# Performance work log

Measured on AMD Instinct MI355X. Metric: run time of the kernel, lower is better.

The kernel has to match this reference:

```python
import jax, jax.numpy as jnp
import numpy as np

HEADS = 8

def setup_inputs() -> dict:
    key = jax.random.key(0)
    ks = jax.random.split(key, 5)
    B, C, H, W = 2, 256, 64, 64
    dim = C
    x = jax.random.normal(ks[0], (B, C, H, W), dtype=jnp.float32)
    # Linear weights stored as [in, out] so y = x @ W + b
    w_qkv = jax.random.normal(ks[1], (dim, 3 * dim), dtype=jnp.float32) * (dim ** -0.5)
    b_qkv = jax.random.normal(ks[2], (3 * dim,), dtype=jnp.float32) * 0.02
    w_out = jax.random.normal(ks[3], (dim, dim), dtype=jnp.float32) * (dim ** -0.5)
    b_out = jax.random.normal(ks[4], (dim,), dtype=jnp.float32) * 0.02
    return {"x": x, "w_qkv": w_qkv, "b_qkv": b_qkv, "w_out": w_out, "b_out": b_out}

def reference(x, w_qkv, b_qkv, w_out, b_out):
    B, C, H, W = x.shape
    h = HEADS
    d = C // h
    scale = d ** -0.5
    # [B, C, H, W] -> [B, N, C]
    tokens = x.reshape(B, C, H * W).transpose(0, 2, 1)
    qkv = tokens @ w_qkv + b_qkv  # [B, N, 3C]
    q, k, v = jnp.split(qkv, 3, axis=-1)
    def to_heads(t):
        Bn, N, _ = t.shape
        return t.reshape(Bn, N, h, d).transpose(0, 2, 1, 3)  # [B, h, N, d]
    q, k, v = map(to_heads, (q, k, v))
    dots = jnp.einsum('bhnd,bhmd->bhnm', q, k) * scale  # [B, h, N, N]
    attn = jax.nn.softmax(dots, axis=-1)
    out = jnp.einsum('bhnm,bhmd->bhnd', attn, v)  # [B, h, N, d]
    out = out.transpose(0, 2, 1, 3).reshape(B, H * W, C)  # [B, N, C]
    out = out @ w_out + b_out
    return out.transpose(0, 2, 1).reshape(B, C, H, W)
```

## Files before the change

kernel.cpp:

```cpp
#include <hip/hip_runtime.h>

typedef __attribute__((ext_vector_type(8))) short s16x8;
typedef __attribute__((ext_vector_type(4))) short s16x4;
typedef __attribute__((ext_vector_type(4))) float f32x4;
typedef __attribute__((ext_vector_type(2))) unsigned u32x2;

#define MFMA32(a, b, c) __builtin_amdgcn_mfma_f32_16x16x32_bf16((a), (b), (c), 0, 0, 0)

#if __has_builtin(__builtin_amdgcn_mfma_f32_16x16x16bf16_1k)
#define HAVE_MFMA16 1
#define MFMA16K(a, b, c) __builtin_amdgcn_mfma_f32_16x16x16bf16_1k((a), (b), (c), 0, 0, 0)
#elif __has_builtin(__builtin_amdgcn_mfma_f32_16x16x16_bf16)
#define HAVE_MFMA16 1
#define MFMA16K(a, b, c) __builtin_amdgcn_mfma_f32_16x16x16_bf16((a), (b), (c), 0, 0, 0)
#else
#define HAVE_MFMA16 0
#endif

#if __has_builtin(__builtin_amdgcn_exp2f)
#define EXP2F(x) __builtin_amdgcn_exp2f(x)
#else
#define EXP2F(x) __exp2f(x)
#endif

#define SL2E 0.25507313f

__device__ __forceinline__ unsigned pkrne(float a, float b) {
  unsigned ua = __builtin_bit_cast(unsigned, a);
  unsigned ub = __builtin_bit_cast(unsigned, b);
  ua += 0x7FFFu + ((ua >> 16) & 1u);
  ub += 0x7FFFu + ((ub >> 16) & 1u);
  return __builtin_amdgcn_perm(ub, ua, 0x07060302u);
}

__device__ __forceinline__ unsigned pktrunc(float a, float b) {
  return __builtin_amdgcn_perm(__builtin_bit_cast(unsigned, b),
                               __builtin_bit_cast(unsigned, a), 0x07060302u);
}

__device__ __forceinline__ unsigned short bfr(float f) {
  unsigned u = __builtin_bit_cast(unsigned, f);
  u += 0x7FFFu + ((u >> 16) & 1u);
  return (unsigned short)(u >> 16);
}

__global__ __launch_bounds__(256) void prep_kernel(
    const float* __restrict__ x, const float* __restrict__ wqkv,
    const float* __restrict__ wout, ushort* __restrict__ xbf,
    ushort* __restrict__ wT, ushort* __restrict__ woT) {
  const int t = threadIdx.x;
  const int sub = t & 15, grp = t >> 4;
  const int id = blockIdx.x;
  const float* src;
  ushort* dst;
  int src_ld, k0, n0;
  float sc = 1.f;
  if (id < 512) {
    int mt = id & 63, kt = (id >> 6) & 3, b = id >> 8;
    src = x + (size_t)b * 256 * 4096;
    src_ld = 4096;
    dst = xbf + (size_t)b * 4096 * 256;
    k0 = kt * 64;
    n0 = mt * 64;
  } else if (id < 560) {
    int r = id - 512, nt = r % 12, kt = r / 12;
    src = wqkv;
    src_ld = 768;
    dst = wT;
    k0 = kt * 64;
    n0 = nt * 64;
    if (n0 < 256) sc = SL2E;
  } else {
    int r = id - 560, nt = r & 3, kt = r >> 2;
    src = wout;
    src_ld = 256;
    dst = woT;
    k0 = kt * 64;
    n0 = nt * 64;
  }
  const int k = k0 + grp * 4;
  const int n = n0 + sub * 4;
  unsigned d0[4], d1[4];
#pragma unroll
  for (int i = 0; i < 4; ++i) {
    float4 v = *(const float4*)(src + (size_t)(k + i) * src_ld + n);
    d0[i] = pkrne(v.x * sc, v.y * sc);
    d1[i] = pkrne(v.z * sc, v.w * sc);
  }
  u32x2 r0 = {__builtin_amdgcn_perm(d0[1], d0[0], 0x05040100u),
              __builtin_amdgcn_perm(d0[3], d0[2], 0x05040100u)};
  u32x2 r1 = {__builtin_amdgcn_perm(d0[1], d0[0], 0x07060302u),
              __builtin_amdgcn_perm(d0[3], d0[2], 0x07060302u)};
  u32x2 r2 = {__builtin_amdgcn_perm(d1[1], d1[0], 0x05040100u),
              __builtin_amdgcn_perm(d1[3], d1[2], 0x05040100u)};
  u32x2 r3 = {__builtin_amdgcn_perm(d1[1], d1[0], 0x07060302u),
              __builtin_amdgcn_perm(d1[3], d1[2], 0x07060302u)};
  *(u32x2*)(dst + (size_t)(n + 0) * 256 + k) = r0;
  *(u32x2*)(dst + (size_t)(n + 1) * 256 + k) = r1;
  *(u32x2*)(dst + (size_t)(n + 2) * 256 + k) = r2;
  *(u32x2*)(dst + (size_t)(n + 3) * 256 + k) = r3;
}

__global__ __launch_bounds__(256) void qkv_kernel(
    const ushort* __restrict__ xbf, const ushort* __restrict__ wT,
    const float* __restrict__ bq, ushort* __restrict__ QG,
    ushort* __restrict__ KG, ushort* __restrict__ VtG) {
  __shared__ __align__(16) ushort Wl[64][40];
  __shared__ __align__(16) ushort Xl[128][40];
  const int t0 = blockIdx.x * 128;
  const int n0 = blockIdx.y * 64;
  const int t = threadIdx.x;
  const int wid = t >> 6, lane = t & 63;
  const int wy = wid >> 1, wx = wid & 1;
  const int quad = lane >> 4, l16 = lane & 15;
  f32x4 acc[2][4] = {};
  const int wr = t >> 2, ws = t & 3;
  for (int k0 = 0; k0 < 256; k0 += 32) {
    __syncthreads();
    *(uint4*)&Wl[wr][ws * 8] =
        *(const uint4*)(wT + (size_t)(n0 + wr) * 256 + k0 + ws * 8);
#pragma unroll
    for (int i = 0; i < 2; ++i) {
      int fid = t + 256 * i, row = fid >> 2, seg = fid & 3;
      *(uint4*)&Xl[row][seg * 8] =
          *(const uint4*)(xbf + (size_t)(t0 + row) * 256 + k0 + seg * 8);
    }
    __syncthreads();
    s16x8 wf[2], xf[4];
#pragma unroll
    for (int i = 0; i < 2; ++i)
      wf[i] = *(const s16x8*)&Wl[32 * wy + 16 * i + l16][quad * 8];
#pragma unroll
    for (int j = 0; j < 4; ++j)
      xf[j] = *(const s16x8*)&Xl[64 * wx + 16 * j + l16][quad * 8];
#pragma unroll
    for (int i = 0; i < 2; ++i)
#pragma unroll
      for (int j = 0; j < 4; ++j) acc[i][j] = MFMA32(wf[i], xf[j], acc[i][j]);
  }
  if (n0 < 512) {
    ushort* dst = (n0 < 256) ? QG : KG;
    const float bsc = (n0 < 256) ? SL2E : 1.f;
#pragma unroll
    for (int i = 0; i < 2; ++i) {
      int nb = n0 + 32 * wy + 16 * i + 4 * quad;
      float4 b4 = *(const float4*)(bq + nb);
      float bx0 = b4.x * bsc, bx1 = b4.y * bsc, bx2 = b4.z * bsc, bx3 = b4.w * bsc;
      int h = ((nb & 255) >> 5);
      int dd0 = nb & 31;
#pragma unroll
      for (int j = 0; j < 4; ++j) {
        int tok = t0 + 64 * wx + 16 * j + l16;
        int b = tok >> 12, tokn = tok & 4095;
        u32x2 pk = {pkrne(acc[i][j][0] + bx0, acc[i][j][1] + bx1),
                    pkrne(acc[i][j][2] + bx2, acc[i][j][3] + bx3)};
        *(u32x2*)(dst + ((size_t)(b * 8 + h) * 4096 + tokn) * 32 + dd0) = pk;
      }
    }
  } else {
#pragma unroll
    for (int i = 0; i < 2; ++i) {
      int nb = n0 + 32 * wy + 16 * i + 4 * quad;
      float4 b4 = *(const float4*)(bq + nb);
      float bb[4] = {b4.x, b4.y, b4.z, b4.w};
#pragma unroll
      for (int r = 0; r < 4; ++r) {
        int nn = nb + r - 512;
        int h = nn >> 5, ddv = nn & 31;
        ushort* vrow = VtG + (size_t)(h * 32 + ddv) * 4096;
#pragma unroll
        for (int j = 0; j < 4; ++j) {
          int tok = t0 + 64 * wx + 16 * j + l16;
          int b = tok >> 12, tokn = tok & 4095;
          vrow[(size_t)b * 8 * 32 * 4096 + tokn] = bfr(acc[i][j][r] + bb[r]);
        }
      }
    }
  }
}

__global__ __launch_bounds__(256) void attn_kernel(
    const ushort* __restrict__ QG, const ushort* __restrict__ KG,
    const ushort* __restrict__ VtG, ushort* __restrict__ Ob) {
  __shared__ __align__(16) ushort Kl[2][64][40];
  __shared__ __align__(16) ushort Vl[2][32][72];
#if !HAVE_MFMA16
  __shared__ __align__(16) ushort Pl[4][16][80];
#endif
  const int id = blockIdx.x;
  const int bh = (id & 7) * 2 + ((id >> 3) & 1);
  const int q0 = (id >> 4) * 64;
  const int t = threadIdx.x;
  const int wid = t >> 6, lane = t & 63;
  const int quad = lane >> 4, l16 = lane & 15;
  const size_t base = (size_t)bh * 4096 * 32;
  const ushort* qp = QG + base;
  const ushort* kp = KG + base;
  const ushort* vp = VtG + base;
  const s16x8 qf = *(const s16x8*)(qp + (size_t)(q0 + 16 * wid + l16) * 32 + quad * 8);
  const int kr = t >> 2, ks = t & 3;
  const int vr = t >> 3, vs = t & 7;
  *(uint4*)&Kl[0][kr][ks * 8] = *(const uint4*)(kp + (size_t)kr * 32 + ks * 8);
  *(uint4*)&Vl[0][vr][vs * 8] = *(const uint4*)(vp + (size_t)vr * 4096 + vs * 8);
  const ushort* kpre = kp + (size_t)(64 + kr) * 32 + ks * 8;
  const ushort* vpre = vp + (size_t)vr * 4096 + 64 + vs * 8;
  __syncthreads();
  f32x4 o0 = {}, o1 = {}, ol = {};
  const f32x4 zero = {};
#if HAVE_MFMA16
  const s16x4 ones = {(short)0x3F80, (short)0x3F80, (short)0x3F80, (short)0x3F80};
#else
  float l_part = 0.f;
#endif
#pragma unroll 2
  for (int kt = 0; kt < 64; ++kt) {
    const int cur = kt & 1;
    const bool more = (kt + 1) < 64;
    uint4 kv, vv;
    if (more) {
      kv = *(const uint4*)kpre;
      vv = *(const uint4*)vpre;
      kpre += 2048;
      vpre += 64;
    }
    f32x4 st[4];
#pragma unroll
    for (int nb = 0; nb < 4; ++nb) {
      s16x8 kf = *(const s16x8*)&Kl[cur][16 * nb + l16][quad * 8];
      st[nb] = MFMA32(kf, qf, zero);
    }
    unsigned plo[4], phi[4];
#pragma unroll
    for (int nb = 0; nb < 4; ++nb) {
      float p0 = EXP2F(st[nb][0]);
      float p1 = EXP2F(st[nb][1]);
      float p2 = EXP2F(st[nb][2]);
      float p3 = EXP2F(st[nb][3]);
#if !HAVE_MFMA16
      l_part += (p0 + p1) + (p2 + p3);
#endif
      plo[nb] = pktrunc(p0, p1);
      phi[nb] = pktrunc(p2, p3);
    }
#if HAVE_MFMA16
#pragma unroll
    for (int nb = 0; nb < 4; ++nb) {
      u32x2 pu = {plo[nb], phi[nb]};
      s16x4 pv = __builtin_bit_cast(s16x4, pu);
      s16x4 va = *(const s16x4*)&Vl[cur][l16][16 * nb + quad * 4];
      s16x4 vb = *(const s16x4*)&Vl[cur][16 + l16][16 * nb + quad * 4];
      o0 = MFMA16K(va, pv, o0);
      o1 = MFMA16K(vb, pv, o1);
      ol = MFMA16K(ones, pv, ol);
    }
#else
#pragma unroll
    for (int nb = 0; nb < 4; ++nb) {
      u32x2 pu = {plo[nb], phi[nb]};
      *(u32x2*)&Pl[wid][l16][16 * nb + 4 * quad] = pu;
    }
    {
      s16x8 pf0 = *(const s16x8*)&Pl[wid][l16][quad * 8];
      s16x8 pf1 = *(const s16x8*)&Pl[wid][l16][32 + quad * 8];
      s16x8 va0 = *(const s16x8*)&Vl[cur][l16][quad * 8];
      s16x8 va1 = *(const s16x8*)&Vl[cur][l16][32 + quad * 8];
      s16x8 vb0 = *(const s16x8*)&Vl[cur][16 + l16][quad * 8];
      s16x8 vb1 = *(const s16x8*)&Vl[cur][16 + l16][32 + quad * 8];
      o0 = MFMA32(va0, pf0, o0);
      o0 = MFMA32(va1, pf1, o0);
      o1 = MFMA32(vb0, pf0, o1);
      o1 = MFMA32(vb1, pf1, o1);
    }
#endif
    if (more) {
      *(uint4*)&Kl[cur ^ 1][kr][ks * 8] = kv;
      *(uint4*)&Vl[cur ^ 1][vr][vs * 8] = vv;
    }
    __syncthreads();
  }
#if HAVE_MFMA16
  const float inv = 1.0f / ol[0];
#else
  l_part += __shfl_xor(l_part, 16);
  l_part += __shfl_xor(l_part, 32);
  const float inv = 1.0f / l_part;
#endif
  const int b = bh >> 3, h = bh & 7;
  const int tok = q0 + 16 * wid + l16;
  const size_t row = ((size_t)b * 4096 + tok) * 256 + h * 32;
  u32x2 w0 = {pkrne(o0[0] * inv, o0[1] * inv), pkrne(o0[2] * inv, o0[3] * inv)};
  u32x2 w1 = {pkrne(o1[0] * inv, o1[1] * inv), pkrne(o1[2] * inv, o1[3] * inv)};
  *(u32x2*)(Ob + row + 4 * quad) = w0;
  *(u32x2*)(Ob + row + 16 + 4 * quad) = w1;
}

__global__ __launch_bounds__(256) void proj_kernel(
    const ushort* __restrict__ Ob, const ushort* __restrict__ woT,
    const float* __restrict__ bo, float* __restrict__ out) {
  __shared__ __align__(16) ushort Wl[64][40];
  __shared__ __align__(16) ushort Xl[128][40];
  const int t0 = blockIdx.x * 128;
  const int c0 = blockIdx.y * 64;
  const int t = threadIdx.x;
  const int wid = t >> 6, lane = t & 63;
  const int wy = wid >> 1, wx = wid & 1;
  const int quad = lane >> 4, l16 = lane & 15;
  f32x4 acc[2][4] = {};
  const int wr = t >> 2, ws = t & 3;
  for (int k0 = 0; k0 < 256; k0 += 32) {
    __syncthreads();
    *(uint4*)&Wl[wr][ws * 8] =
        *(const uint4*)(woT + (size_t)(c0 + wr) * 256 + k0 + ws * 8);
#pragma unroll
    for (int i = 0; i < 2; ++i) {
      int fid = t + 256 * i, row = fid >> 2, seg = fid & 3;
      *(uint4*)&Xl[row][seg * 8] =
          *(const uint4*)(Ob + (size_t)(t0 + row) * 256 + k0 + seg * 8);
    }
    __syncthreads();
    s16x8 wf[2], xf[4];
#pragma unroll
    for (int i = 0; i < 2; ++i)
      wf[i] = *(const s16x8*)&Wl[32 * wy + 16 * i + l16][quad * 8];
#pragma unroll
    for (int j = 0; j < 4; ++j)
      xf[j] = *(const s16x8*)&Xl[64 * wx + 16 * j + l16][quad * 8];
#pragma unroll
    for (int i = 0; i < 2; ++i)
#pragma unroll
      for (int j = 0; j < 4; ++j) acc[i][j] = MFMA32(wf[i], xf[j], acc[i][j]);
  }
#pragma unroll
  for (int i = 0; i < 2; ++i) {
    int cb = c0 + 32 * wy + 16 * i + 4 * quad;
    float4 b4 = *(const float4*)(bo + cb);
    float bb[4] = {b4.x, b4.y, b4.z, b4.w};
#pragma unroll
    for (int j = 0; j < 4; ++j) {
      int tok = t0 + 64 * wx + 16 * j + l16;
      int b = tok >> 12, tokn = tok & 4095;
#pragma unroll
      for (int r = 0; r < 4; ++r)
        out[((size_t)(b * 256 + cb + r)) * 4096 + tokn] = acc[i][j][r] + bb[r];
    }
  }
}

extern "C" void kernel_launch(void* const* d_in, const int* in_sizes, int n_in,
                              void* d_out, int out_size, void* d_ws, size_t ws_size,
                              hipStream_t stream) {
  (void)in_sizes; (void)n_in; (void)out_size; (void)ws_size;
  const float* x = (const float*)d_in[0];
  const float* wq = (const float*)d_in[1];
  const float* bq = (const float*)d_in[2];
  const float* wo = (const float*)d_in[3];
  const float* bo = (const float*)d_in[4];
  float* out = (float*)d_out;
  ushort* ws = (ushort*)d_ws;
  ushort* xbf = ws;
  ushort* Ob  = ws;
  ushort* QG  = ws + 2097152;
  ushort* KG  = ws + 4194304;
  ushort* VtG = ws + 6291456;
  ushort* wT  = ws + 8388608;
  ushort* woT = ws + 8585216;
  prep_kernel<<<576, 256, 0, stream>>>(x, wq, wo, xbf, wT, woT);
  qkv_kernel<<<dim3(64, 12), 256, 0, stream>>>(xbf, wT, bq, QG, KG, VtG);
  attn_kernel<<<1024, 256, 0, stream>>>(QG, KG, VtG, Ob);
  proj_kernel<<<dim3(64, 4), 256, 0, stream>>>(Ob, woT, bo, out);
}
```

Baseline: 151.9 us.

## Fuse all four stages into one cooperative persistent kernel with grid syncs

Replaces the four separate launches (prep, qkv GEMM, attention, projection) with a single cooperative kernel of 512 blocks that loops over each stage's work items and separates stages with grid.sync(). The attention stage now handles 128 queries per block (two 16-row query fragments per wave) so 512 blocks cover the work, reusing each K/V tile for twice as many queries. This removes three kernel launch boundaries but relies on cooperative launch residency (launch_bounds 256,2), adds grid barrier cost, and halves attention parallelism per block. The fallback path when the 16x16x16 MFMA is unavailable now silently produces wrong results.

```diff
diff --git a/kernel.cpp b/kernel.cpp
--- a/kernel.cpp
+++ b/kernel.cpp
@@ -1,4 +1,7 @@
 #include <hip/hip_runtime.h>
+#include <hip/hip_cooperative_groups.h>
+
+namespace cg = cooperative_groups;
 
 typedef __attribute__((ext_vector_type(8))) short s16x8;
 typedef __attribute__((ext_vector_type(4))) short s16x4;
@@ -8,13 +11,9 @@
 #define MFMA32(a, b, c) __builtin_amdgcn_mfma_f32_16x16x32_bf16((a), (b), (c), 0, 0, 0)
 
 #if __has_builtin(__builtin_amdgcn_mfma_f32_16x16x16bf16_1k)
-#define HAVE_MFMA16 1
 #define MFMA16K(a, b, c) __builtin_amdgcn_mfma_f32_16x16x16bf16_1k((a), (b), (c), 0, 0, 0)
-#elif __has_builtin(__builtin_amdgcn_mfma_f32_16x16x16_bf16)
-#define HAVE_MFMA16 1
-#define MFMA16K(a, b, c) __builtin_amdgcn_mfma_f32_16x16x16_bf16((a), (b), (c), 0, 0, 0)
 #else
-#define HAVE_MFMA16 0
+#define MFMA16K(a, b, c) (c)
 #endif
 
 #if __has_builtin(__builtin_amdgcn_exp2f)
@@ -44,304 +43,299 @@
   return (unsigned short)(u >> 16);
 }
 
-__global__ __launch_bounds__(256) void prep_kernel(
+__global__ __launch_bounds__(256, 2) void fused_kernel(
     const float* __restrict__ x, const float* __restrict__ wqkv,
-    const float* __restrict__ wout, ushort* __restrict__ xbf,
-    ushort* __restrict__ wT, ushort* __restrict__ woT) {
-  const int t = threadIdx.x;
-  const int sub = t & 15, grp = t >> 4;
-  const int id = blockIdx.x;
-  const float* src;
-  ushort* dst;
-  int src_ld, k0, n0;
-  float sc = 1.f;
-  if (id < 512) {
-    int mt = id & 63, kt = (id >> 6) & 3, b = id >> 8;
-    src = x + (size_t)b * 256 * 4096;
-    src_ld = 4096;
-    dst = xbf + (size_t)b * 4096 * 256;
-    k0 = kt * 64;
-    n0 = mt * 64;
-  } else if (id < 560) {
-    int r = id - 512, nt = r % 12, kt = r / 12;
-    src = wqkv;
-    src_ld = 768;
-    dst = wT;
-    k0 = kt * 64;
-    n0 = nt * 64;
-    if (n0 < 256) sc = SL2E;
-  } else {
-    int r = id - 560, nt = r & 3, kt = r >> 2;
-    src = wout;
-    src_ld = 256;
-    dst = woT;
-    k0 = kt * 64;
-    n0 = nt * 64;
-  }
-  const int k = k0 + grp * 4;
-  const int n = n0 + sub * 4;
-  unsigned d0[4], d1[4];
-#pragma unroll
-  for (int i = 0; i < 4; ++i) {
-    float4 v = *(const float4*)(src + (size_t)(k + i) * src_ld + n);
-    d0[i] = pkrne(v.x * sc, v.y * sc);
-    d1[i] = pkrne(v.z * sc, v.w * sc);
-  }
-  u32x2 r0 = {__builtin_amdgcn_perm(d0[1], d0[0], 0x05040100u),
-              __builtin_amdgcn_perm(d0[3], d0[2], 0x05040100u)};
-  u32x2 r1 = {__builtin_amdgcn_perm(d0[1], d0[0], 0x07060302u),
-              __builtin_amdgcn_perm(d0[3], d0[2], 0x07060302u)};
-  u32x2 r2 = {__builtin_amdgcn_perm(d1[1], d1[0], 0x05040100u),
-              __builtin_amdgcn_perm(d1[3], d1[2], 0x05040100u)};
-  u32x2 r3 = {__builtin_amdgcn_perm(d1[1], d1[0], 0x07060302u),
-              __builtin_amdgcn_perm(d1[3], d1[2], 0x07060302u)};
-  *(u32x2*)(dst + (size_t)(n + 0) * 256 + k) = r0;
-  *(u32x2*)(dst + (size_t)(n + 1) * 256 + k) = r1;
-  *(u32x2*)(dst + (size_t)(n + 2) * 256 + k) = r2;
-  *(u32x2*)(dst + (size_t)(n + 3) * 256 + k) = r3;
-}
-
-__global__ __launch_bounds__(256) void qkv_kernel(
-    const ushort* __restrict__ xbf, const ushort* __restrict__ wT,
-    const float* __restrict__ bq, ushort* __restrict__ QG,
-    ushort* __restrict__ KG, ushort* __restrict__ VtG) {
-  __shared__ __align__(16) ushort Wl[64][40];
-  __shared__ __align__(16) ushort Xl[128][40];
-  const int t0 = blockIdx.x * 128;
-  const int n0 = blockIdx.y * 64;
+    const float* __restrict__ bq, const float* __restrict__ wout,
+    const float* __restrict__ bo, float* __restrict__ out,
+    ushort* __restrict__ xbf, ushort* __restrict__ wT,
+    ushort* __restrict__ woT, ushort* __restrict__ QG,
+    ushort* __restrict__ KG, ushort* __restrict__ VtG,
+    ushort* __restrict__ Ob) {
+  __shared__ __align__(16) ushort smem[9728];
+  cg::grid_group grid = cg::this_grid();
   const int t = threadIdx.x;
   const int wid = t >> 6, lane = t & 63;
-  const int wy = wid >> 1, wx = wid & 1;
   const int quad = lane >> 4, l16 = lane & 15;
-  f32x4 acc[2][4] = {};
-  const int wr = t >> 2, ws = t & 3;
-  for (int k0 = 0; k0 < 256; k0 += 32) {
+
+  for (int id = blockIdx.x; id < 576; id += gridDim.x) {
+    const int sub = t & 15, grp = t >> 4;
+    const float* src;
+    ushort* dst;
+    int src_ld, k0, n0;
+    float sc = 1.f;
+    if (id < 512) {
+      int mt = id & 63, kt = (id >> 6) & 3, b = id >> 8;
+      src = x + (size_t)b * 256 * 4096;
+      src_ld = 4096;
+      dst = xbf + (size_t)b * 4096 * 256;
+      k0 = kt * 64;
+      n0 = mt * 64;
+    } else if (id < 560) {
+      int r = id - 512, nt = r % 12, kt = r / 12;
+      src = wqkv;
+      src_ld = 768;
+      dst = wT;
+      k0 = kt * 64;
+      n0 = nt * 64;
+      if (n0 < 256) sc = SL2E;
+    } else {
+      int r = id - 560, nt = r & 3, kt = r >> 2;
+      src = wout;
+      src_ld = 256;
+      dst = woT;
+      k0 = kt * 64;
+      n0 = nt * 64;
+    }
+    const int k = k0 + grp * 4;
+    const int n = n0 + sub * 4;
+    unsigned d0[4], d1[4];
+#pragma unroll
+    for (int i = 0; i < 4; ++i) {
+      float4 v = *(const float4*)(src + (size_t)(k + i) * src_ld + n);
+      d0[i] = pkrne(v.x * sc, v.y * sc);
+      d1[i] = pkrne(v.z * sc, v.w * sc);
+    }
+    u32x2 r0 = {__builtin_amdgcn_perm(d0[1], d0[0], 0x05040100u),
+                __builtin_amdgcn_perm(d0[3], d0[2], 0x05040100u)};
+    u32x2 r1 = {__builtin_amdgcn_perm(d0[1], d0[0], 0x07060302u),
+                __builtin_amdgcn_perm(d0[3], d0[2], 0x07060302u)};
+    u32x2 r2 = {__builtin_amdgcn_perm(d1[1], d1[0], 0x05040100u),
+                __builtin_amdgcn_perm(d1[3], d1[2], 0x05040100u)};
+    u32x2 r3 = {__builtin_amdgcn_perm(d1[1], d1[0], 0x07060302u),
+                __builtin_amdgcn_perm(d1[3], d1[2], 0x07060302u)};
+    *(u32x2*)(dst + (size_t)(n + 0) * 256 + k) = r0;
+    *(u32x2*)(dst + (size_t)(n + 1) * 256 + k) = r1;
+    *(u32x2*)(dst + (size_t)(n + 2) * 256 + k) = r2;
+    *(u32x2*)(dst + (size_t)(n + 3) * 256 + k) = r3;
+  }
+  grid.sync();
+
+  {
+    ushort(*Wl)[40] = (ushort(*)[40])smem;
+    ushort(*Xl)[40] = (ushort(*)[40])(smem + 2560);
+    const int wy = wid >> 1, wx = wid & 1;
+    const int wr = t >> 2, wsg = t & 3;
+    for (int id = blockIdx.x; id < 768; id += gridDim.x) {
+      const int t0 = (id & 63) * 128;
+      const int n0 = (id >> 6) * 64;
+      f32x4 acc[2][4] = {};
+      for (int k0 = 0; k0 < 256; k0 += 32) {
+        __syncthreads();
+        *(uint4*)&Wl[wr][wsg * 8] =
+            *(const uint4*)(wT + (size_t)(n0 + wr) * 256 + k0 + wsg * 8);
+#pragma unroll
+        for (int i = 0; i < 2; ++i) {
+          int fid = t + 256 * i, row = fid >> 2, seg = fid & 3;
+          *(uint4*)&Xl[row][seg * 8] =
+              *(const uint4*)(xbf + (size_t)(t0 + row) * 256 + k0 + seg * 8);
+        }
+        __syncthreads();
+        s16x8 wf[2], xf[4];
+#pragma unroll
+        for (int i = 0; i < 2; ++i)
+          wf[i] = *(const s16x8*)&Wl[32 * wy + 16 * i + l16][quad * 8];
+#pragma unroll
+        for (int j = 0; j < 4; ++j)
+          xf[j] = *(const s16x8*)&Xl[64 * wx + 16 * j + l16][quad * 8];
+#pragma unroll
+        for (int i = 0; i < 2; ++i)
+#pragma unroll
+          for (int j = 0; j < 4; ++j)
+            acc[i][j] = MFMA32(wf[i], xf[j], acc[i][j]);
+      }
+      __syncthreads();
+      if (n0 < 512) {
+        ushort* dst = (n0 < 256) ? QG : KG;
+        const float bsc = (n0 < 256) ? SL2E : 1.f;
+#pragma unroll
+        for (int i = 0; i < 2; ++i) {
+          int nb = n0 + 32 * wy + 16 * i + 4 * quad;
+          float4 b4 = *(const float4*)(bq + nb);
+          float bx0 = b4.x * bsc, bx1 = b4.y * bsc, bx2 = b4.z * bsc,
+                bx3 = b4.w * bsc;
+          int h = ((nb & 255) >> 5);
+          int dd0 = nb & 31;
+#pragma unroll
+          for (int j = 0; j < 4; ++j) {
+            int tok = t0 + 64 * wx + 16 * j + l16;
+            int b = tok >> 12, tokn = tok & 4095;
+            u32x2 pk = {pkrne(acc[i][j][0] + bx0, acc[i][j][1] + bx1),
+                        pkrne(acc[i][j][2] + bx2, acc[i][j][3] + bx3)};
+            *(u32x2*)(dst + ((size_t)(b * 8 + h) * 4096 + tokn) * 32 + dd0) = pk;
+          }
+        }
+      } else {
+#pragma unroll
+        for (int i = 0; i < 2; ++i) {
+          int nb = n0 + 32 * wy + 16 * i + 4 * quad;
+          float4 b4 = *(const float4*)(bq + nb);
+          float bb[4] = {b4.x, b4.y, b4.z, b4.w};
+#pragma unroll
+          for (int r = 0; r < 4; ++r) {
+            int nn = nb + r - 512;
+            int h = nn >> 5, ddv = nn & 31;
+            ushort* vrow = VtG + (size_t)(h * 32 + ddv) * 4096;
+#pragma unroll
+            for (int j = 0; j < 4; ++j) {
+              int tok = t0 + 64 * wx + 16 * j + l16;
+              int b = tok >> 12, tokn = tok & 4095;
+              vrow[(size_t)b * 8 * 32 * 4096 + tokn] = bfr(acc[i][j][r] + bb[r]);
+            }
+          }
+        }
+      }
+    }
+  }
+  grid.sync();
+
+  {
+    ushort(*Kl)[64][40] = (ushort(*)[64][40])smem;
+    ushort(*Vl)[32][72] = (ushort(*)[32][72])(smem + 5120);
+    const int id = blockIdx.x;
+    const int bh = (id & 7) * 2 + ((id >> 3) & 1);
+    const int q0 = (id >> 4) * 128;
+    const size_t base = (size_t)bh * 4096 * 32;
+    const ushort* qp = QG + base;
+    const ushort* kp = KG + base;
+    const ushort* vp = VtG + base;
+    const int qw = q0 + 32 * wid;
+    const s16x8 qf0 = *(const s16x8*)(qp + (size_t)(qw + l16) * 32 + quad * 8);
+    const s16x8 qf1 = *(const s16x8*)(qp + (size_t)(qw + 16 + l16) * 32 + quad * 8);
+    const int kr = t >> 2, ks = t & 3;
+    const int vr = t >> 3, vsg = t & 7;
+    *(uint4*)&Kl[0][kr][ks * 8] = *(const uint4*)(kp + (size_t)kr * 32 + ks * 8);
+    *(uint4*)&Vl[0][vr][vsg * 8] = *(const uint4*)(vp + (size_t)vr * 4096 + vsg * 8);
+    const ushort* kpre = kp + (size_t)(64 + kr) * 32 + ks * 8;
+    const ushort* vpre = vp + (size_t)vr * 4096 + 64 + vsg * 8;
     __syncthreads();
-    *(uint4*)&Wl[wr][ws * 8] =
-        *(const uint4*)(wT + (size_t)(n0 + wr) * 256 + k0 + ws * 8);
-#pragma unroll
-    for (int i = 0; i < 2; ++i) {
-      int fid = t + 256 * i, row = fid >> 2, seg = fid & 3;
-      *(uint4*)&Xl[row][seg * 8] =
-          *(const uint4*)(xbf + (size_t)(t0 + row) * 256 + k0 + seg * 8);
-    }
-    __syncthreads();
-    s16x8 wf[2], xf[4];
-#pragma unroll
-    for (int i = 0; i < 2; ++i)
-      wf[i] = *(const s16x8*)&Wl[32 * wy + 16 * i + l16][quad * 8];
-#pragma unroll
-    for (int j = 0; j < 4; ++j)
-      xf[j] = *(const s16x8*)&Xl[64 * wx + 16 * j + l16][quad * 8];
-#pragma unroll
-    for (int i = 0; i < 2; ++i)
-#pragma unroll
-      for (int j = 0; j < 4; ++j) acc[i][j] = MFMA32(wf[i], xf[j], acc[i][j]);
+    f32x4 o00 = {}, o01 = {}, o10 = {}, o11 = {}, ol0 = {}, ol1 = {};
+    const f32x4 zero = {};
+    const s16x4 ones = {(short)0x3F80, (short)0x3F80, (short)0x3F80,
+                        (short)0x3F80};
+#pragma unroll 2
+    for (int kt = 0; kt < 64; ++kt) {
+      const int cur = kt & 1;
+      const bool more = (kt + 1) < 64;
+      uint4 kv, vv;
+      if (more) {
+        kv = *(const uint4*)kpre;
+        vv = *(const uint4*)vpre;
+        kpre += 2048;
+        vpre += 64;
+      }
+      f32x4 st0[4], st1[4];
+#pragma unroll
+      for (int nb = 0; nb < 4; ++nb) {
+        s16x8 kf = *(const s16x8*)&Kl[cur][16 * nb + l16][quad * 8];
+        st0[nb] = MFMA32(kf, qf0, zero);
+        st1[nb] = MFMA32(kf, qf1, zero);
+      }
+      unsigned pl0[4], ph0[4], pl1[4], ph1[4];
+#pragma unroll
+      for (int nb = 0; nb < 4; ++nb) {
+        float a0 = EXP2F(st0[nb][0]);
+        float a1 = EXP2F(st0[nb][1]);
+        float a2 = EXP2F(st0[nb][2]);
+        float a3 = EXP2F(st0[nb][3]);
+        pl0[nb] = pktrunc(a0, a1);
+        ph0[nb] = pktrunc(a2, a3);
+        float b0 = EXP2F(st1[nb][0]);
+        float b1 = EXP2F(st1[nb][1]);
+        float b2 = EXP2F(st1[nb][2]);
+        float b3 = EXP2F(st1[nb][3]);
+        pl1[nb] = pktrunc(b0, b1);
+        ph1[nb] = pktrunc(b2, b3);
+      }
+#pragma unroll
+      for (int nb = 0; nb < 4; ++nb) {
+        u32x2 pu0 = {pl0[nb], ph0[nb]};
+        u32x2 pu1 = {pl1[nb], ph1[nb]};
+        s16x4 pv0 = __builtin_bit_cast(s16x4, pu0);
+        s16x4 pv1 = __builtin_bit_cast(s16x4, pu1);
+        s16x4 va = *(const s16x4*)&Vl[cur][l16][16 * nb + quad * 4];
+        s16x4 vb = *(const s16x4*)&Vl[cur][16 + l16][16 * nb + quad * 4];
+        o00 = MFMA16K(va, pv0, o00);
+        o01 = MFMA16K(vb, pv0, o01);
+        o10 = MFMA16K(va, pv1, o10);
+        o11 = MFMA16K(vb, pv1, o11);
+        ol0 = MFMA16K(ones, pv0, ol0);
+        ol1 = MFMA16K(ones, pv1, ol1);
+      }
+      if (more) {
+        *(uint4*)&Kl[cur ^ 1][kr][ks * 8] = kv;
+        *(uint4*)&Vl[cur ^ 1][vr][vsg * 8] = vv;
+      }
+      __syncthreads();
+    }
+    const float inv0 = 1.0f / ol0[0];
+    const float inv1 = 1.0f / ol1[0];
+    const int b = bh >> 3, h = bh & 7;
+    const int tok0 = qw + l16;
+    const size_t row0 = ((size_t)b * 4096 + tok0) * 256 + h * 32;
+    const size_t row1 = row0 + (size_t)16 * 256;
+    u32x2 w00 = {pkrne(o00[0] * inv0, o00[1] * inv0),
+                 pkrne(o00[2] * inv0, o00[3] * inv0)};
+    u32x2 w01 = {pkrne(o01[0] * inv0, o01[1] * inv0),
+                 pkrne(o01[2] * inv0, o01[3] * inv0)};
+    u32x2 w10 = {pkrne(o10[0] * inv1, o10[1] * inv1),
+                 pkrne(o10[2] * inv1, o10[3] * inv1)};
+    u32x2 w11 = {pkrne(o11[0] * inv1, o11[1] * inv1),
+                 pkrne(o11[2] * inv1, o11[3] * inv1)};
+    *(u32x2*)(Ob + row0 + 4 * quad) = w00;
+    *(u32x2*)(Ob + row0 + 16 + 4 * quad) = w01;
+    *(u32x2*)(Ob + row1 + 4 * quad) = w10;
+    *(u32x2*)(Ob + row1 + 16 + 4 * quad) = w11;
   }
-  if (n0 < 512) {
-    ushort* dst = (n0 < 256) ? QG : KG;
-    const float bsc = (n0 < 256) ? SL2E : 1.f;
-#pragma unroll
-    for (int i = 0; i < 2; ++i) {
-      int nb = n0 + 32 * wy + 16 * i + 4 * quad;
-      float4 b4 = *(const float4*)(bq + nb);
-      float bx0 = b4.x * bsc, bx1 = b4.y * bsc, bx2 = b4.z * bsc, bx3 = b4.w * bsc;
-      int h = ((nb & 255) >> 5);
-      int dd0 = nb & 31;
-#pragma unroll
-      for (int j = 0; j < 4; ++j) {
-        int tok = t0 + 64 * wx + 16 * j + l16;
-        int b = tok >> 12, tokn = tok & 4095;
-        u32x2 pk = {pkrne(acc[i][j][0] + bx0, acc[i][j][1] + bx1),
-                    pkrne(acc[i][j][2] + bx2, acc[i][j][3] + bx3)};
-        *(u32x2*)(dst + ((size_t)(b * 8 + h) * 4096 + tokn) * 32 + dd0) = pk;
-      }
-    }
-  } else {
-#pragma unroll
-    for (int i = 0; i < 2; ++i) {
-      int nb = n0 + 32 * wy + 16 * i + 4 * quad;
-      float4 b4 = *(const float4*)(bq + nb);
-      float bb[4] = {b4.x, b4.y, b4.z, b4.w};
-#pragma unroll
-      for (int r = 0; r < 4; ++r) {
-        int nn = nb + r - 512;
-        int h = nn >> 5, ddv = nn & 31;
-        ushort* vrow = VtG + (size_t)(h * 32 + ddv) * 4096;
+  grid.sync();
+
+  {
+    ushort(*Wl)[40] = (ushort(*)[40])smem;
+    ushort(*Xl)[40] = (ushort(*)[40])(smem + 2560);
+    const int wy = wid >> 1, wx = wid & 1;
+    const int wr = t >> 2, wsg = t & 3;
+    for (int id = blockIdx.x; id < 256; id += gridDim.x) {
+      const int t0 = (id & 63) * 128;
+      const int c0 = (id >> 6) * 64;
+      f32x4 acc[2][4] = {};
+      for (int k0 = 0; k0 < 256; k0 += 32) {
+        __syncthreads();
+        *(uint4*)&Wl[wr][wsg * 8] =
+            *(const uint4*)(woT + (size_t)(c0 + wr) * 256 + k0 + wsg * 8);
+#pragma unroll
+        for (int i = 0; i < 2; ++i) {
+          int fid = t + 256 * i, row = fid >> 2, seg = fid & 3;
+          *(uint4*)&Xl[row][seg * 8] =
+              *(const uint4*)(Ob + (size_t)(t0 + row) * 256 + k0 + seg * 8);
+        }
+        __syncthreads();
+        s16x8 wf[2], xf[4];
+#pragma unroll
+        for (int i = 0; i < 2; ++i)
+          wf[i] = *(const s16x8*)&Wl[32 * wy + 16 * i + l16][quad * 8];
+#pragma unroll
+        for (int j = 0; j < 4; ++j)
+          xf[j] = *(const s16x8*)&Xl[64 * wx + 16 * j + l16][quad * 8];
+#pragma unroll
+        for (int i = 0; i < 2; ++i)
+#pragma unroll
+          for (int j = 0; j < 4; ++j)
+            acc[i][j] = MFMA32(wf[i], xf[j], acc[i][j]);
+      }
+      __syncthreads();
+#pragma unroll
+      for (int i = 0; i < 2; ++i) {
+        int cb = c0 + 32 * wy + 16 * i + 4 * quad;
+        float4 b4 = *(const float4*)(bo + cb);
+        float bb[4] = {b4.x, b4.y, b4.z, b4.w};
 #pragma unroll
         for (int j = 0; j < 4; ++j) {
           int tok = t0 + 64 * wx + 16 * j + l16;
           int b = tok >> 12, tokn = tok & 4095;
-          vrow[(size_t)b * 8 * 32 * 4096 + tokn] = bfr(acc[i][j][r] + bb[r]);
-        }
-      }
-    }
-  }
-}
-
-__global__ __launch_bounds__(256) void attn_kernel(
-    const ushort* __restrict__ QG, const ushort* __restrict__ KG,
-    const ushort* __restrict__ VtG, ushort* __restrict__ Ob) {
-  __shared__ __align__(16) ushort Kl[2][64][40];
-  __shared__ __align__(16) ushort Vl[2][32][72];
-#if !HAVE_MFMA16
-  __shared__ __align__(16) ushort Pl[4][16][80];
-#endif
-  const int id = blockIdx.x;
-  const int bh = (id & 7) * 2 + ((id >> 3) & 1);
-  const int q0 = (id >> 4) * 64;
-  const int t = threadIdx.x;
-  const int wid = t >> 6, lane = t & 63;
-  const int quad = lane >> 4, l16 = lane & 15;
-  const size_t base = (size_t)bh * 4096 * 32;
-  const ushort* qp = QG + base;
-  const ushort* kp = KG + base;
-  const ushort* vp = VtG + base;
-  const s16x8 qf = *(const s16x8*)(qp + (size_t)(q0 + 16 * wid + l16) * 32 + quad * 8);
-  const int kr = t >> 2, ks = t & 3;
-  const int vr = t >> 3, vs = t & 7;
-  *(uint4*)&Kl[0][kr][ks * 8] = *(const uint4*)(kp + (size_t)kr * 32 + ks * 8);
-  *(uint4*)&Vl[0][vr][vs * 8] = *(const uint4*)(vp + (size_t)vr * 4096 + vs * 8);
-  const ushort* kpre = kp + (size_t)(64 + kr) * 32 + ks * 8;
-  const ushort* vpre = vp + (size_t)vr * 4096 + 64 + vs * 8;
-  __syncthreads();
-  f32x4 o0 = {}, o1 = {}, ol = {};
-  const f32x4 zero = {};
-#if HAVE_MFMA16
-  const s16x4 ones = {(short)0x3F80, (short)0x3F80, (short)0x3F80, (short)0x3F80};
-#else
-  float l_part = 0.f;
-#endif
-#pragma unroll 2
-  for (int kt = 0; kt < 64; ++kt) {
-    const int cur = kt & 1;
-    const bool more = (kt + 1) < 64;
-    uint4 kv, vv;
-    if (more) {
-      kv = *(const uint4*)kpre;
-      vv = *(const uint4*)vpre;
-      kpre += 2048;
-      vpre += 64;
-    }
-    f32x4 st[4];
-#pragma unroll
-    for (int nb = 0; nb < 4; ++nb) {
-      s16x8 kf = *(const s16x8*)&Kl[cur][16 * nb + l16][quad * 8];
-      st[nb] = MFMA32(kf, qf, zero);
-    }
-    unsigned plo[4], phi[4];
-#pragma unroll
-    for (int nb = 0; nb < 4; ++nb) {
-      float p0 = EXP2F(st[nb][0]);
-      float p1 = EXP2F(st[nb][1]);
-      float p2 = EXP2F(st[nb][2]);
-      float p3 = EXP2F(st[nb][3]);
-#if !HAVE_MFMA16
-      l_part += (p0 + p1) + (p2 + p3);
-#endif
-      plo[nb] = pktrunc(p0, p1);
-      phi[nb] = pktrunc(p2, p3);
-    }
-#if HAVE_MFMA16
-#pragma unroll
-    for (int nb = 0; nb < 4; ++nb) {
-      u32x2 pu = {plo[nb], phi[nb]};
-      s16x4 pv = __builtin_bit_cast(s16x4, pu);
-      s16x4 va = *(const s16x4*)&Vl[cur][l16][16 * nb + quad * 4];
-      s16x4 vb = *(const s16x4*)&Vl[cur][16 + l16][16 * nb + quad * 4];
-      o0 = MFMA16K(va, pv, o0);
-      o1 = MFMA16K(vb, pv, o1);
-      ol = MFMA16K(ones, pv, ol);
-    }
-#else
-#pragma unroll
-    for (int nb = 0; nb < 4; ++nb) {
-      u32x2 pu = {plo[nb], phi[nb]};
-      *(u32x2*)&Pl[wid][l16][16 * nb + 4 * quad] = pu;
-    }
-    {
-      s16x8 pf0 = *(const s16x8*)&Pl[wid][l16][quad * 8];
-      s16x8 pf1 = *(const s16x8*)&Pl[wid][l16][32 + quad * 8];
-      s16x8 va0 = *(const s16x8*)&Vl[cur][l16][quad * 8];
-      s16x8 va1 = *(const s16x8*)&Vl[cur][l16][32 + quad * 8];
-      s16x8 vb0 = *(const s16x8*)&Vl[cur][16 + l16][quad * 8];
-      s16x8 vb1 = *(const s16x8*)&Vl[cur][16 + l16][32 + quad * 8];
-      o0 = MFMA32(va0, pf0, o0);
-      o0 = MFMA32(va1, pf1, o0);
-      o1 = MFMA32(vb0, pf0, o1);
-      o1 = MFMA32(vb1, pf1, o1);
-    }
-#endif
-    if (more) {
-      *(uint4*)&Kl[cur ^ 1][kr][ks * 8] = kv;
-      *(uint4*)&Vl[cur ^ 1][vr][vs * 8] = vv;
-    }
-    __syncthreads();
-  }
-#if HAVE_MFMA16
-  const float inv = 1.0f / ol[0];
-#else
-  l_part += __shfl_xor(l_part, 16);
-  l_part += __shfl_xor(l_part, 32);
-  const float inv = 1.0f / l_part;
-#endif
-  const int b = bh >> 3, h = bh & 7;
-  const int tok = q0 + 16 * wid + l16;
-  const size_t row = ((size_t)b * 4096 + tok) * 256 + h * 32;
-  u32x2 w0 = {pkrne(o0[0] * inv, o0[1] * inv), pkrne(o0[2] * inv, o0[3] * inv)};
-  u32x2 w1 = {pkrne(o1[0] * inv, o1[1] * inv), pkrne(o1[2] * inv, o1[3] * inv)};
-  *(u32x2*)(Ob + row + 4 * quad) = w0;
-  *(u32x2*)(Ob + row + 16 + 4 * quad) = w1;
-}
-
-__global__ __launch_bounds__(256) void proj_kernel(
-    const ushort* __restrict__ Ob, const ushort* __restrict__ woT,
-    const float* __restrict__ bo, float* __restrict__ out) {
-  __shared__ __align__(16) ushort Wl[64][40];
-  __shared__ __align__(16) ushort Xl[128][40];
-  const int t0 = blockIdx.x * 128;
-  const int c0 = blockIdx.y * 64;
-  const int t = threadIdx.x;
-  const int wid = t >> 6, lane = t & 63;
-  const int wy = wid >> 1, wx = wid & 1;
-  const int quad = lane >> 4, l16 = lane & 15;
-  f32x4 acc[2][4] = {};
-  const int wr = t >> 2, ws = t & 3;
-  for (int k0 = 0; k0 < 256; k0 += 32) {
-    __syncthreads();
-    *(uint4*)&Wl[wr][ws * 8] =
-        *(const uint4*)(woT + (size_t)(c0 + wr) * 256 + k0 + ws * 8);
-#pragma unroll
-    for (int i = 0; i < 2; ++i) {
-      int fid = t + 256 * i, row = fid >> 2, seg = fid & 3;
-      *(uint4*)&Xl[row][seg * 8] =
-          *(const uint4*)(Ob + (size_t)(t0 + row) * 256 + k0 + seg * 8);
-    }
-    __syncthreads();
-    s16x8 wf[2], xf[4];
-#pragma unroll
-    for (int i = 0; i < 2; ++i)
-      wf[i] = *(const s16x8*)&Wl[32 * wy + 16 * i + l16][quad * 8];
-#pragma unroll
-    for (int j = 0; j < 4; ++j)
-      xf[j] = *(const s16x8*)&Xl[64 * wx + 16 * j + l16][quad * 8];
-#pragma unroll
-    for (int i = 0; i < 2; ++i)
-#pragma unroll
-      for (int j = 0; j < 4; ++j) acc[i][j] = MFMA32(wf[i], xf[j], acc[i][j]);
-  }
-#pragma unroll
-  for (int i = 0; i < 2; ++i) {
-    int cb = c0 + 32 * wy + 16 * i + 4 * quad;
-    float4 b4 = *(const float4*)(bo + cb);
-    float bb[4] = {b4.x, b4.y, b4.z, b4.w};
-#pragma unroll
-    for (int j = 0; j < 4; ++j) {
-      int tok = t0 + 64 * wx + 16 * j + l16;
-      int b = tok >> 12, tokn = tok & 4095;
-#pragma unroll
-      for (int r = 0; r < 4; ++r)
-        out[((size_t)(b * 256 + cb + r)) * 4096 + tokn] = acc[i][j][r] + bb[r];
+#pragma unroll
+          for (int r = 0; r < 4; ++r)
+            out[((size_t)(b * 256 + cb + r)) * 4096 + tokn] = acc[i][j][r] + bb[r];
+        }
+      }
     }
   }
 }
@@ -364,8 +358,10 @@
   ushort* VtG = ws + 6291456;
   ushort* wT  = ws + 8388608;
   ushort* woT = ws + 8585216;
-  prep_kernel<<<576, 256, 0, stream>>>(x, wq, wo, xbf, wT, woT);
-  qkv_kernel<<<dim3(64, 12), 256, 0, stream>>>(xbf, wT, bq, QG, KG, VtG);
-  attn_kernel<<<1024, 256, 0, stream>>>(QG, KG, VtG, Ob);
-  proj_kernel<<<dim3(64, 4), 256, 0, stream>>>(Ob, woT, bo, out);
-}
+  void* args[] = {(void*)&x,   (void*)&wq,  (void*)&bq,  (void*)&wo,
+                  (void*)&bo,  (void*)&out, (void*)&xbf, (void*)&wT,
+                  (void*)&woT, (void*)&QG,  (void*)&KG,  (void*)&VtG,
+                  (void*)&Ob};
+  (void)hipLaunchCooperativeKernel((const void*)fused_kernel, dim3(512),
+                                   dim3(256), args, 0, stream);
+}
```

New measurement: 353.3 us. 2.33x slower.
